# Optimization experiments

Hardware: AMD Instinct MI355X
Metric: run time of the kernel (lower is better)

## Reference

```python
import jax, jax.numpy as jnp
import numpy as np

E, D, H = 1024, 64, 16   # embed_dim, head_dim, num_heads
B, L = 8, 4096


def _ln(x, g, b, eps=1e-5):
    m = jnp.mean(x, axis=-1, keepdims=True)
    v = jnp.var(x, axis=-1, keepdims=True)
    return (x - m) / jnp.sqrt(v + eps) * g + b


def setup_inputs() -> dict:
    key = jax.random.key(0)
    ks = jax.random.split(key, 10)
    s_e = 1.0 / np.sqrt(E)
    s_d = 1.0 / np.sqrt(D)
    f32 = jnp.float32
    return {
        "emb": jax.random.normal(ks[0], (B, L, E), f32),
        # per-head linears stacked on a leading head axis
        "Wa": jax.random.normal(ks[1], (H, E, D), f32) * s_e,
        "ba": jnp.zeros((H, D), f32),
        "Wb": jax.random.normal(ks[2], (H, E, D), f32) * s_e,
        "bb": jnp.zeros((H, D), f32),
        "Wc": jax.random.normal(ks[3], (H, D, D), f32) * s_d,
        "bc": jnp.zeros((H, D), f32),
        "head_w": jnp.ones((H,), f32),
        "hn_g": jnp.ones((H, D), f32),
        "hn_b": jnp.zeros((H, D), f32),
        "Wd": jax.random.normal(ks[4], (E, D), f32) * s_e,
        "bd": jnp.zeros((D,), f32),
        "W1": jax.random.normal(ks[5], (D, 4 * D), f32) * s_d,
        "b1": jnp.zeros((4 * D,), f32),
        "W2": jax.random.normal(ks[6], (4 * D, D), f32) * (1.0 / np.sqrt(4 * D)),
        "b2": jnp.zeros((D,), f32),
        "Wp": jax.random.normal(ks[7], (D, D), f32) * s_d,
        "bp": jnp.zeros((D,), f32),
        "ng": jnp.ones((D,), f32),
        "nb": jnp.zeros((D,), f32),
    }


def reference(emb, Wa, ba, Wb, bb, Wc, bc, head_w, hn_g, hn_b,
              Wd, bd, W1, b1, W2, b2, Wp, bp, ng, nb):
    b_sz, seq_len, _ = emb.shape
    n_heads, d_head = ba.shape

    # gates depend only on x_t -> precompute for all t, all heads  [B,L,H,D]
    a = jnp.tanh(jnp.einsum('ble,hed->blhd', emb, Wa) + ba)
    bt = jnp.einsum('ble,hed->blhd', emb, Wb) + bb

    # linear recurrence h_t = a_t * h_{t-1} + b_t over time
    a_t = jnp.moveaxis(a, 1, 0)    # [L,B,H,D]
    b_t = jnp.moveaxis(bt, 1, 0)

    def step(h, ab):
        at, btt = ab
        h = at * h + btt
        return h, h

    h0 = jnp.zeros((b_sz, n_heads, d_head), emb.dtype)
    _, hs = jax.lax.scan(step, h0, (a_t, b_t))
    hs = jnp.moveaxis(hs, 0, 1)    # [B,L,H,D]

    dx = emb @ Wd + bd             # [B,L,D] shared D(x_t)

    out = jnp.einsum('blhd,hde->blhe', hs, Wc) + bc + dx[:, :, None, :]
    out = _ln(out, hn_g, hn_b)     # per-head LayerNorm, gamma/beta [H,D]

    sum_heads = dx + jnp.einsum('h,blhd->bld', head_w, out)
    z = sum_heads / n_heads

    u = z + _ln(z, ng, nb)
    ffn = jax.nn.gelu(u @ W1 + b1, approximate=False) @ W2 + b2
    h_out = u + ffn
    return h_out @ Wp + bp
```

## Files before the change

### kernel.cpp

```cpp
#include <hip/hip_runtime.h>
#include <hip/hip_bf16.h>
#include <math.h>
#include <stdint.h>

#define E_DIM 1024
#define D_DIM 64
#define H_DIM 16
#define B_SZ  8
#define L_SEQ 4096
#define M_TOK (B_SZ * L_SEQ)
#define NCAT  2112
#define NPAD  2304
#define CHUNK 64
#define NCHUNK (L_SEQ / CHUNK)

typedef float  f32x4  __attribute__((ext_vector_type(4)));
typedef __bf16 bf16x8 __attribute__((ext_vector_type(8)));
typedef __bf16 bf16x4 __attribute__((ext_vector_type(4)));

__device__ __forceinline__ float tanh_fast(float v) {
  float vc = fminf(fmaxf(v, -12.f), 12.f);
  float ex = __expf(vc + vc);
  return (ex - 1.f) / (ex + 1.f);
}
__device__ __forceinline__ void load_lds16(const void* g, void* l) {
  __builtin_amdgcn_global_load_lds(
      (const __attribute__((address_space(1))) void*)g,
      (__attribute__((address_space(3))) void*)l, 16, 0, 0);
}

__global__ __launch_bounds__(256) void cast_emb(const float* __restrict__ in,
                                                bf16x4* __restrict__ out) {
  int i = blockIdx.x * 256 + threadIdx.x;
  float4 v = ((const float4*)in)[i];
  bf16x4 o;
  o[0] = (__bf16)v.x; o[1] = (__bf16)v.y; o[2] = (__bf16)v.z; o[3] = (__bf16)v.w;
  out[i] = o;
}

__global__ __launch_bounds__(256) void pack_w(
    const float* __restrict__ Wa, const float* __restrict__ ba,
    const float* __restrict__ Wb, const float* __restrict__ bb,
    const float* __restrict__ Wd, const float* __restrict__ bd,
    __bf16* __restrict__ wcat, float* __restrict__ bias) {
  int gid = blockIdx.x * 256 + threadIdx.x;
  int n = gid >> 10, k = gid & 1023;
  float w, bv;
  if (n < 1024) {
    int h = n >> 6, d = n & 63;
    w = Wa[((h << 10) | k) * 64 + d]; bv = ba[n];
  } else if (n < 2048) {
    int nn = n - 1024; int h = nn >> 6, d = nn & 63;
    w = Wb[((h << 10) | k) * 64 + d]; bv = bb[nn];
  } else if (n < NCAT) {
    int d = n - 2048;
    w = Wd[k * 64 + d];  bv = bd[d];
  } else { w = 0.f; bv = 0.f; }
  wcat[n * 1024 + k] = (__bf16)w;
  if (k == 0) bias[n] = bv;
}

__global__ __launch_bounds__(256) void pack_ffnw(
    const float* __restrict__ W1, const float* __restrict__ W2,
    const float* __restrict__ Wp,
    __bf16* __restrict__ g_w1t, __bf16* __restrict__ g_w2t,
    __bf16* __restrict__ g_wpt) {
  int idx = blockIdx.x * 256 + threadIdx.x;
  if (idx < 16384) {
    int k = idx >> 8, n = idx & 255;
    g_w1t[n * 72 + k] = (__bf16)W1[idx];
  } else if (idx < 32768) {
    int j = idx - 16384; int k = j >> 6, n = j & 63;
    g_w2t[n * 256 + (((k >> 3) ^ (n & 7)) << 3) + (k & 7)] = (__bf16)W2[j];
  } else {
    int j = idx - 32768; int k = j >> 6, n = j & 63;
    g_wpt[n * 72 + k] = (__bf16)Wp[j];
  }
}

__global__ __launch_bounds__(256) void pack_wct(const float* __restrict__ Wc,
                                                __bf16* __restrict__ wct) {
  int idx = blockIdx.x * 256 + threadIdx.x;
  int h = idx >> 12, e = (idx >> 6) & 63, d = idx & 63;
  wct[idx] = (__bf16)Wc[h * 4096 + d * 64 + e];
}

__global__ __launch_bounds__(512, 2) void gemm_fused(
    const __bf16* __restrict__ A, const __bf16* __restrict__ Wt,
    const float* __restrict__ bias,
    __bf16* __restrict__ abuf, __bf16* __restrict__ bbuf, float* __restrict__ dxbuf) {
  __shared__ __bf16 lds[65536];
  const int id = blockIdx.x;
  const int wg = (id & 7) * 144 + (id >> 3);
  const int mt = wg / 9, nt = wg % 9;
  const int m0 = mt * 256, n0 = nt * 256;
  const int t = threadIdx.x;
  const int w = t >> 6, l = t & 63;
  const int wr = w >> 2, wc = w & 3;
  const int q = l >> 4, c16 = l & 15;
  const int cp = q ^ ((c16 >> 1) & 3);
  const int srow = l >> 2;
  const int schk = (l & 3) ^ ((l >> 3) & 3);

  f32x4 acc[8][4];
#pragma unroll
  for (int i = 0; i < 8; ++i)
#pragma unroll
    for (int j = 0; j < 4; ++j) acc[i][j] = (f32x4)(0.f);

  auto stage = [&](int H) {
    int th = H >> 1, isB = H & 1, slot = th & 3;
    const __bf16* src = isB ? Wt : A;
    int base0 = isB ? n0 : m0;
    int ldsbase = (isB ? 32768 : 0) + slot * 8192;
#pragma unroll
    for (int r = 0; r < 2; ++r) {
      int rw = r * 128 + w * 16;
      load_lds16(src + (size_t)(base0 + rw + srow) * 1024 + th * 32 + schk * 8,
                 &lds[ldsbase + rw * 32]);
    }
  };

  auto tile_phases = [&](int tt, bool sA, bool sB) {
    const int slot = tt & 3;
    const __bf16* Asl = lds + slot * 8192;
    const __bf16* Bsl = lds + 32768 + slot * 8192;
    bf16x8 bfr[4], af[4];
#pragma unroll
    for (int j = 0; j < 4; ++j)
      bfr[j] = *(const bf16x8*)(Bsl + (wc * 64 + j * 16 + c16) * 32 + cp * 8);
#pragma unroll
    for (int i = 0; i < 4; ++i)
      af[i] = *(const bf16x8*)(Asl + (wr * 128 + i * 16 + c16) * 32 + cp * 8);
    if (sA) stage(2 * tt + 5);
    __builtin_amdgcn_s_setprio(1);
#pragma unroll
    for (int i = 0; i < 4; ++i)
#pragma unroll
      for (int j = 0; j < 4; ++j)
        acc[i][j] = __builtin_amdgcn_mfma_f32_16x16x32_bf16(af[i], bfr[j], acc[i][j], 0, 0, 0);
    __builtin_amdgcn_s_setprio(0);
    asm volatile("s_barrier" ::: "memory");
#pragma unroll
    for (int i = 0; i < 4; ++i)
      af[i] = *(const bf16x8*)(Asl + (wr * 128 + (4 + i) * 16 + c16) * 32 + cp * 8);
    if (sB) stage(2 * tt + 6);
    __builtin_amdgcn_s_setprio(1);
#pragma unroll
    for (int i = 0; i < 4; ++i)
#pragma unroll
      for (int j = 0; j < 4; ++j)
        acc[4 + i][j] = __builtin_amdgcn_mfma_f32_16x16x32_bf16(af[i], bfr[j], acc[4 + i][j], 0, 0, 0);
    __builtin_amdgcn_s_setprio(0);
  };

  stage(0); stage(1); stage(2); stage(3); stage(4);
  asm volatile("s_waitcnt vmcnt(6)" ::: "memory");
  asm volatile("s_barrier" ::: "memory");

#pragma unroll 1
  for (int tt = 0; tt < 29; ++tt) {
    tile_phases(tt, true, true);
    asm volatile("s_waitcnt vmcnt(6)" ::: "memory");
    asm volatile("s_barrier" ::: "memory");
  }
  tile_phases(29, true, false);
  asm volatile("s_waitcnt vmcnt(4)" ::: "memory");
  asm volatile("s_barrier" ::: "memory");
  tile_phases(30, false, false);
  asm volatile("s_waitcnt vmcnt(0)" ::: "memory");
  asm volatile("s_barrier" ::: "memory");
  tile_phases(31, false, false);

#pragma unroll
  for (int j = 0; j < 4; ++j) {
    int n = n0 + wc * 64 + j * 16 + c16;
    if (n >= NCAT) continue;
    float bv = bias[n];
#pragma unroll
    for (int i = 0; i < 8; ++i) {
      int mbase = m0 + wr * 128 + i * 16 + q * 4;
#pragma unroll
      for (int r = 0; r < 4; ++r) {
        float v = acc[i][j][r] + bv;
        int m = mbase + r;
        if (n < 1024)            abuf[(size_t)m * 1024 + n] = (__bf16)tanh_fast(v);
        else if (n < 2048)       bbuf[(size_t)m * 1024 + (n - 1024)] = (__bf16)v;
        else                     dxbuf[m * 64 + (n - 2048)] = v;
      }
    }
  }
}

__global__ __launch_bounds__(256) void scan_local_bf(
    __bf16* __restrict__ abuf, __bf16* __restrict__ bbuf,
    float* __restrict__ cA, float* __restrict__ cH) {
  int bc = blockIdx.x;
  int n4 = threadIdx.x * 4;
  size_t base = (size_t)bc * CHUNK * 1024 + n4;
  float p[4] = {1.f, 1.f, 1.f, 1.f}, h[4] = {0.f, 0.f, 0.f, 0.f};
#pragma unroll 4
  for (int s = 0; s < CHUNK; ++s) {
    size_t idx = base + (size_t)s * 1024;
    bf16x4 av = *(const bf16x4*)(abuf + idx);
    bf16x4 bv = *(const bf16x4*)(bbuf + idx);
    bf16x4 po, ho;
#pragma unroll
    for (int i = 0; i < 4; ++i) {
      float a = (float)av[i];
      p[i] *= a;
      h[i] = fmaf(a, h[i], (float)bv[i]);
      po[i] = (__bf16)p[i];
      ho[i] = (__bf16)h[i];
    }
    *(bf16x4*)(abuf + idx) = po;
    *(bf16x4*)(bbuf + idx) = ho;
  }
  int ci = bc * 1024 + n4;
  float4 pv = {p[0], p[1], p[2], p[3]};
  float4 hv = {h[0], h[1], h[2], h[3]};
  *(float4*)(cA + ci) = pv;
  *(float4*)(cH + ci) = hv;
}

__global__ __launch_bounds__(256) void scan_carry(
    const float* __restrict__ cA, const float* __restrict__ cH, float* __restrict__ cIn) {
  int gid = blockIdx.x * 256 + threadIdx.x;
  int n = gid & 1023, b = gid >> 10;
  float carry = 0.f;
  for (int c = 0; c < NCHUNK; ++c) {
    int idx = (b * NCHUNK + c) * 1024 + n;
    cIn[idx] = carry;
    carry = fmaf(cA[idx], carry, cH[idx]);
  }
}

__global__ __launch_bounds__(256) void heads_mfma(
    const __bf16* __restrict__ ahat, const __bf16* __restrict__ hloc,
    const float* __restrict__ dxbuf, const float* __restrict__ cIn,
    const __bf16* __restrict__ wct, const float* __restrict__ bch,
    const float* __restrict__ head_w, const float* __restrict__ hng,
    const float* __restrict__ hnb, const float* __restrict__ ng,
    const float* __restrict__ nbv, float* __restrict__ ubuf) {
  __shared__ float carryS[1024];
  const int tid = threadIdx.x, w = tid >> 6, l = tid & 63;
  const int q = l >> 4, c16 = l & 15;
  const int m0 = blockIdx.x * 64;
  const int b = m0 >> 12, c = (m0 & 4095) >> 6;
  const int cb = (b * NCHUNK + c) * 1024;
  ((float4*)carryS)[tid] = ((const float4*)(cIn + cb))[tid];
  __syncthreads();

  const size_t arow = (size_t)(m0 + w * 16 + c16) * 1024;

  float dxr[4][4];
#pragma unroll
  for (int j = 0; j < 4; ++j)
#pragma unroll
    for (int r = 0; r < 4; ++r)
      dxr[j][r] = dxbuf[(m0 + w * 16 + q * 4 + r) * 64 + j * 16 + c16];

  f32x4 accum[4];
#pragma unroll
  for (int j = 0; j < 4; ++j) accum[j] = (f32x4)(0.f);

  for (int h = 0; h < H_DIM; ++h) {
    bf16x8 af[2];
#pragma unroll
    for (int ks = 0; ks < 2; ++ks) {
      int dbase = h * 64 + ks * 32 + q * 8;
      bf16x8 av = *(const bf16x8*)(ahat + arow + dbase);
      bf16x8 hv = *(const bf16x8*)(hloc + arow + dbase);
      float4 cv0 = *(const float4*)(carryS + dbase);
      float4 cv1 = *(const float4*)(carryS + dbase + 4);
      bf16x8 hf;
      hf[0] = (__bf16)fmaf((float)av[0], cv0.x, (float)hv[0]);
      hf[1] = (__bf16)fmaf((float)av[1], cv0.y, (float)hv[1]);
      hf[2] = (__bf16)fmaf((float)av[2], cv0.z, (float)hv[2]);
      hf[3] = (__bf16)fmaf((float)av[3], cv0.w, (float)hv[3]);
      hf[4] = (__bf16)fmaf((float)av[4], cv1.x, (float)hv[4]);
      hf[5] = (__bf16)fmaf((float)av[5], cv1.y, (float)hv[5]);
      hf[6] = (__bf16)fmaf((float)av[6], cv1.z, (float)hv[6]);
      hf[7] = (__bf16)fmaf((float)av[7], cv1.w, (float)hv[7]);
      af[ks] = hf;
    }
    f32x4 acc[4];
#pragma unroll
    for (int j = 0; j < 4; ++j) acc[j] = (f32x4)(0.f);
#pragma unroll
    for (int ks = 0; ks < 2; ++ks)
#pragma unroll
      for (int j = 0; j < 4; ++j) {
        bf16x8 bf = *(const bf16x8*)(wct + h * 4096 + (j * 16 + c16) * 64 + ks * 32 + q * 8);
        acc[j] = __builtin_amdgcn_mfma_f32_16x16x32_bf16(af[ks], bf, acc[j], 0, 0, 0);
      }
    float hw = head_w[h];
    float g4[4], be4[4], bb4[4];
#pragma unroll
    for (int j = 0; j < 4; ++j) {
      int nh = h * 64 + j * 16 + c16;
      g4[j] = hng[nh]; bb4[j] = hnb[nh]; be4[j] = bch[nh];
    }
#pragma unroll
    for (int r = 0; r < 4; ++r) {
      float v0 = acc[0][r] + be4[0] + dxr[0][r];
      float v1 = acc[1][r] + be4[1] + dxr[1][r];
      float v2 = acc[2][r] + be4[2] + dxr[2][r];
      float v3 = acc[3][r] + be4[3] + dxr[3][r];
      float s  = (v0 + v1) + (v2 + v3);
      float s2 = fmaf(v0, v0, fmaf(v1, v1, fmaf(v2, v2, v3 * v3)));
#pragma unroll
      for (int off = 1; off < 16; off <<= 1) {
        s  += __shfl_xor(s, off, 64);
        s2 += __shfl_xor(s2, off, 64);
      }
      float mean = s * (1.f / 64.f);
      float var  = fmaf(s2, 1.f / 64.f, -mean * mean);
      float inv  = rsqrtf(fmaxf(var, 0.f) + 1e-5f);
      accum[0][r] = fmaf(hw, fmaf((v0 - mean) * inv, g4[0], bb4[0]), accum[0][r]);
      accum[1][r] = fmaf(hw, fmaf((v1 - mean) * inv, g4[1], bb4[1]), accum[1][r]);
      accum[2][r] = fmaf(hw, fmaf((v2 - mean) * inv, g4[2], bb4[2]), accum[2][r]);
      accum[3][r] = fmaf(hw, fmaf((v3 - mean) * inv, g4[3], bb4[3]), accum[3][r]);
    }
  }
  float ng4[4], nb4[4];
#pragma unroll
  for (int j = 0; j < 4; ++j) { ng4[j] = ng[j * 16 + c16]; nb4[j] = nbv[j * 16 + c16]; }
#pragma unroll
  for (int r = 0; r < 4; ++r) {
    float z0 = (dxr[0][r] + accum[0][r]) * (1.f / 16.f);
    float z1 = (dxr[1][r] + accum[1][r]) * (1.f / 16.f);
    float z2 = (dxr[2][r] + accum[2][r]) * (1.f / 16.f);
    float z3 = (dxr[3][r] + accum[3][r]) * (1.f / 16.f);
    float s  = (z0 + z1) + (z2 + z3);
    float s2 = fmaf(z0, z0, fmaf(z1, z1, fmaf(z2, z2, z3 * z3)));
#pragma unroll
    for (int off = 1; off < 16; off <<= 1) {
      s  += __shfl_xor(s, off, 64);
      s2 += __shfl_xor(s2, off, 64);
    }
    float mean = s * (1.f / 64.f);
    float var  = fmaf(s2, 1.f / 64.f, -mean * mean);
    float inv  = rsqrtf(fmaxf(var, 0.f) + 1e-5f);
    int mrow = (m0 + w * 16 + q * 4 + r) * 64;
    ubuf[mrow + 0 * 16 + c16] = z0 + fmaf((z0 - mean) * inv, ng4[0], nb4[0]);
    ubuf[mrow + 1 * 16 + c16] = z1 + fmaf((z1 - mean) * inv, ng4[1], nb4[1]);
    ubuf[mrow + 2 * 16 + c16] = z2 + fmaf((z2 - mean) * inv, ng4[2], nb4[2]);
    ubuf[mrow + 3 * 16 + c16] = z3 + fmaf((z3 - mean) * inv, ng4[3], nb4[3]);
  }
}

__global__ __launch_bounds__(256) void ffn_mfma(
    const float* __restrict__ ubuf,
    const __bf16* __restrict__ g_w1t, const __bf16* __restrict__ g_w2t,
    const __bf16* __restrict__ g_wpt,
    const float* __restrict__ b1, const float* __restrict__ b2,
    const float* __restrict__ bp, float* __restrict__ out) {
  __shared__ __bf16 pool[32768];
  const int tid = threadIdx.x, w = tid >> 6, l = tid & 63;
  const int q = l >> 4, c16 = l & 15;
  const int m0 = blockIdx.x * 64;
  __bf16* Us  = pool;
  __bf16* W1T = pool + 4608;
  __bf16* T1S = pool;
  __bf16* W2T = pool + 16384;
  __bf16* HoS = pool;
  __bf16* WpT = pool + 4608;

#pragma unroll
  for (int r = 0; r < 16; ++r) {
    int idx = r * 256 + tid, m = idx >> 6, e = idx & 63;
    Us[m * 72 + e] = (__bf16)ubuf[(size_t)(m0 + m) * 64 + e];
  }
#pragma unroll
  for (int r = 0; r < 9; ++r)
    load_lds16(g_w1t + (size_t)(r * 256 + tid) * 8,
               (char*)pool + 9216 + (r * 256 + w * 64) * 16);
  __syncthreads();

  f32x4 acc1[16];
#pragma unroll
  for (int j = 0; j < 16; ++j) acc1[j] = (f32x4)(0.f);
#pragma unroll
  for (int ks = 0; ks < 2; ++ks) {
    bf16x8 a = *(const bf16x8*)(Us + (w * 16 + c16) * 72 + ks * 32 + q * 8);
#pragma unroll
    for (int j = 0; j < 16; ++j) {
      bf16x8 b = *(const bf16x8*)(W1T + (j * 16 + c16) * 72 + ks * 32 + q * 8);
      acc1[j] = __builtin_amdgcn_mfma_f32_16x16x32_bf16(a, b, acc1[j], 0, 0, 0);
    }
  }
  __syncthreads();

#pragma unroll
  for (int r = 0; r < 8; ++r)
    load_lds16(g_w2t + (size_t)(r * 256 + tid) * 8,
               (char*)pool + 32768 + (r * 256 + w * 64) * 16);
#pragma unroll
  for (int j = 0; j < 16; ++j) {
    int n = j * 16 + c16;
    float bv = b1[n];
#pragma unroll
    for (int rr = 0; rr < 4; ++rr) {
      int m = w * 16 + q * 4 + rr;
      float x = acc1[j][rr] + bv;
      float g = 0.5f * x * (1.f + erff(x * 0.70710678118654752f));
      T1S[m * 256 + (((n >> 3) ^ (m & 7)) << 3) + (n & 7)] = (__bf16)g;
    }
  }
  __syncthreads();

  f32x4 acc2[4];
#pragma unroll
  for (int j = 0; j < 4; ++j) acc2[j] = (f32x4)(0.f);
  const int arow2 = w * 16 + c16;
#pragma unroll
  for (int ks = 0; ks < 8; ++ks) {
    bf16x8 a = *(const bf16x8*)(T1S + arow2 * 256 + (((ks * 4 + q) ^ (arow2 & 7)) << 3));
#pragma unroll
    for (int j = 0; j < 4; ++j) {
      int brow = j * 16 + c16;
      bf16x8 b = *(const bf16x8*)(W2T + brow * 256 + (((ks * 4 + q) ^ (brow & 7)) << 3));
      acc2[j] = __builtin_amdgcn_mfma_f32_16x16x32_bf16(a, b, acc2[j], 0, 0, 0);
    }
  }
  __syncthreads();

#pragma unroll
  for (int r = 0; r < 2; ++r)
    load_lds16(g_wpt + (size_t)(r * 256 + tid) * 8,
               (char*)pool + 9216 + (r * 256 + w * 64) * 16);
  if (tid < 64)
    load_lds16(g_wpt + (size_t)(512 + tid) * 8, (char*)pool + 9216 + 512 * 16);
#pragma unroll
  for (int j = 0; j < 4; ++j) {
    int e = j * 16 + c16;
    float bv = b2[e];
#pragma unroll
    for (int rr = 0; rr < 4; ++rr) {
      int m = w * 16 + q * 4 + rr;
      float hres = acc2[j][rr] + bv + ubuf[(size_t)(m0 + m) * 64 + e];
      HoS[m * 72 + e] = (__bf16)hres;
    }
  }
  __syncthreads();

  f32x4 acc3[4];
#pragma unroll
  for (int j = 0; j < 4; ++j) acc3[j] = (f32x4)(0.f);
#pragma unroll
  for (int ks = 0; ks < 2; ++ks) {
    bf16x8 a = *(const bf16x8*)(HoS + (w * 16 + c16) * 72 + ks * 32 + q * 8);
#pragma unroll
    for (int j = 0; j < 4; ++j) {
      bf16x8 b = *(const bf16x8*)(WpT + (j * 16 + c16) * 72 + ks * 32 + q * 8);
      acc3[j] = __builtin_amdgcn_mfma_f32_16x16x32_bf16(a, b, acc3[j], 0, 0, 0);
    }
  }
#pragma unroll
  for (int j = 0; j < 4; ++j) {
    int e = j * 16 + c16;
    float bv = bp[e];
#pragma unroll
    for (int rr = 0; rr < 4; ++rr) {
      int m = w * 16 + q * 4 + rr;
      out[(size_t)(m0 + m) * 64 + e] = acc3[j][rr] + bv;
    }
  }
}

extern "C" void kernel_launch(void* const* d_in, const int* in_sizes, int n_in,
                              void* d_out, int out_size, void* d_ws, size_t ws_size,
                              hipStream_t stream) {
  const float* emb    = (const float*)d_in[0];
  const float* Wa     = (const float*)d_in[1];
  const float* ba     = (const float*)d_in[2];
  const float* Wb     = (const float*)d_in[3];
  const float* bb     = (const float*)d_in[4];
  const float* Wc     = (const float*)d_in[5];
  const float* bc     = (const float*)d_in[6];
  const float* head_w = (const float*)d_in[7];
  const float* hn_g   = (const float*)d_in[8];
  const float* hn_b   = (const float*)d_in[9];
  const float* Wd     = (const float*)d_in[10];
  const float* bd     = (const float*)d_in[11];
  const float* W1     = (const float*)d_in[12];
  const float* b1     = (const float*)d_in[13];
  const float* W2     = (const float*)d_in[14];
  const float* b2     = (const float*)d_in[15];
  const float* Wp     = (const float*)d_in[16];
  const float* bp     = (const float*)d_in[17];
  const float* ng     = (const float*)d_in[18];
  const float* nb     = (const float*)d_in[19];
  float* out = (float*)d_out;

  char* wsp = (char*)d_ws;
  size_t off = 0;
  auto alloc = [&](size_t bytes) -> char* {
    char* p = wsp + off;
    off += (bytes + 255) & ~(size_t)255;
    return p;
  };
  __bf16* embh  = (__bf16*)alloc((size_t)M_TOK * E_DIM * 2);
  __bf16* wcat  = (__bf16*)alloc((size_t)NPAD * E_DIM * 2);
  float*  bias  = (float*)alloc((size_t)NPAD * 4);
  __bf16* abuf  = (__bf16*)alloc((size_t)M_TOK * 1024 * 2);
  __bf16* bbuf  = (__bf16*)alloc((size_t)M_TOK * 1024 * 2);
  float*  dxbuf = (float*)alloc((size_t)M_TOK * 64 * 4);
  float*  cA    = (float*)alloc((size_t)512 * 1024 * 4);
  float*  cH    = (float*)alloc((size_t)512 * 1024 * 4);
  float*  cIn   = (float*)alloc((size_t)512 * 1024 * 4);
  float*  ubuf  = (float*)alloc((size_t)M_TOK * 64 * 4);
  __bf16* g_w1t = (__bf16*)alloc((size_t)256 * 72 * 2);
  __bf16* g_w2t = (__bf16*)alloc((size_t)64 * 256 * 2);
  __bf16* g_wpt = (__bf16*)alloc((size_t)64 * 72 * 2);
  __bf16* wct   = (__bf16*)alloc((size_t)H_DIM * 64 * 64 * 2);

  cast_emb<<<dim3(32768), dim3(256), 0, stream>>>(emb, (bf16x4*)embh);
  pack_w<<<dim3(9216), dim3(256), 0, stream>>>(Wa, ba, Wb, bb, Wd, bd, wcat, bias);
  pack_ffnw<<<dim3(144), dim3(256), 0, stream>>>(W1, W2, Wp, g_w1t, g_w2t, g_wpt);
  pack_wct<<<dim3(256), dim3(256), 0, stream>>>(Wc, wct);
  gemm_fused<<<dim3(1152), dim3(512), 0, stream>>>(embh, wcat, bias, abuf, bbuf, dxbuf);
  scan_local_bf<<<dim3(512), dim3(256), 0, stream>>>(abuf, bbuf, cA, cH);
  scan_carry<<<dim3(32), dim3(256), 0, stream>>>(cA, cH, cIn);
  heads_mfma<<<dim3(512), dim3(256), 0, stream>>>(abuf, bbuf, dxbuf, cIn, wct, bc,
                                                  head_w, hn_g, hn_b, ng, nb, ubuf);
  ffn_mfma<<<dim3(512), dim3(256), 0, stream>>>(ubuf, g_w1t, g_w2t, g_wpt,
                                                b1, b2, bp, out);
}
```

Before: 600.5 us.

## Restructure fused GEMM main loop to K=64 tiles with four-phase double buffering

Reworks the LDS staging of the big fused projection GEMM. The K-tile grows from 32 to 64 with an 8-way XOR swizzle, and the buffers go from a 4-slot ring to double buffering split into half-tiles. Each K step runs as four phases that interleave half-tile global-to-LDS loads with MFMA on two row blocks, and each phase has explicit barriers and lgkmcnt/vmcnt waits. The aim is fewer loop iterations and better overlap of loads with MFMA, at the cost of more barriers per tile and a more fragile wait-count schedule.

```diff
diff --git a/kernel.cpp b/kernel.cpp
--- a/kernel.cpp
+++ b/kernel.cpp
@@ -98,9 +98,8 @@
   const int w = t >> 6, l = t & 63;
   const int wr = w >> 2, wc = w & 3;
   const int q = l >> 4, c16 = l & 15;
-  const int cp = q ^ ((c16 >> 1) & 3);
-  const int srow = l >> 2;
-  const int schk = (l & 3) ^ ((l >> 3) & 3);
+  const int cxor = c16 & 7;
+  const int schk = (l & 7) ^ ((l >> 3) & 7);
 
   f32x4 acc[8][4];
 #pragma unroll
@@ -108,69 +107,77 @@
 #pragma unroll
     for (int j = 0; j < 4; ++j) acc[i][j] = (f32x4)(0.f);
 
-  auto stage = [&](int H) {
-    int th = H >> 1, isB = H & 1, slot = th & 3;
+  auto stage = [&](int kt, int isB, int h) {
     const __bf16* src = isB ? Wt : A;
-    int base0 = isB ? n0 : m0;
-    int ldsbase = (isB ? 32768 : 0) + slot * 8192;
-#pragma unroll
-    for (int r = 0; r < 2; ++r) {
-      int rw = r * 128 + w * 16;
-      load_lds16(src + (size_t)(base0 + rw + srow) * 1024 + th * 32 + schk * 8,
-                 &lds[ldsbase + rw * 32]);
-    }
+    const int base0 = (isB ? n0 : m0) + h * 128 + w * 16;
+    __bf16* dst = lds + (isB ? 32768 : 0) + (((kt & 1) << 1) + h) * 8192 + w * 1024;
+#pragma unroll
+    for (int r = 0; r < 2; ++r)
+      load_lds16(src + (size_t)(base0 + r * 8 + (l >> 3)) * 1024 + kt * 64 + schk * 8,
+                 dst + r * 512);
   };
 
-  auto tile_phases = [&](int tt, bool sA, bool sB) {
-    const int slot = tt & 3;
-    const __bf16* Asl = lds + slot * 8192;
-    const __bf16* Bsl = lds + 32768 + slot * 8192;
-    bf16x8 bfr[4], af[4];
-#pragma unroll
-    for (int j = 0; j < 4; ++j)
-      bfr[j] = *(const bf16x8*)(Bsl + (wc * 64 + j * 16 + c16) * 32 + cp * 8);
-#pragma unroll
-    for (int i = 0; i < 4; ++i)
-      af[i] = *(const bf16x8*)(Asl + (wr * 128 + i * 16 + c16) * 32 + cp * 8);
-    if (sA) stage(2 * tt + 5);
+  auto ldA = [&](int d, int i, int ks) -> bf16x8 {
+    return *(const bf16x8*)(lds + ((d << 1) + wr) * 8192 + (i * 16 + c16) * 64 +
+                            (((ks << 2) + q) ^ cxor) * 8);
+  };
+  auto ldB = [&](int d, int j, int ks) -> bf16x8 {
+    return *(const bf16x8*)(lds + 32768 + ((d << 1) + (wc >> 1)) * 8192 +
+                            ((wc & 1) * 64 + j * 16 + c16) * 64 +
+                            (((ks << 2) + q) ^ cxor) * 8);
+  };
+
+  bf16x8 bfr[4][2];
+
+  auto phase = [&](int d, int i0, bool loadB, bool do_stage, int skt, int sisB,
+                   int sh, int wait) {
+    if (loadB) {
+#pragma unroll
+      for (int j = 0; j < 4; ++j) {
+        bfr[j][0] = ldB(d, j, 0);
+        bfr[j][1] = ldB(d, j, 1);
+      }
+    }
+    bf16x8 a00 = ldA(d, i0, 0), a01 = ldA(d, i0, 1);
+    bf16x8 a10 = ldA(d, i0 + 1, 0), a11 = ldA(d, i0 + 1, 1);
+    if (do_stage) stage(skt, sisB, sh);
+    __builtin_amdgcn_sched_barrier(0);
+    __builtin_amdgcn_s_barrier();
+    asm volatile("s_waitcnt lgkmcnt(0)" ::: "memory");
+    __builtin_amdgcn_sched_barrier(0);
     __builtin_amdgcn_s_setprio(1);
 #pragma unroll
-    for (int i = 0; i < 4; ++i)
+    for (int ks = 0; ks < 2; ++ks) {
+      const bf16x8 a0 = ks ? a01 : a00;
+      const bf16x8 a1 = ks ? a11 : a10;
 #pragma unroll
       for (int j = 0; j < 4; ++j)
-        acc[i][j] = __builtin_amdgcn_mfma_f32_16x16x32_bf16(af[i], bfr[j], acc[i][j], 0, 0, 0);
+        acc[i0][j] = __builtin_amdgcn_mfma_f32_16x16x32_bf16(a0, bfr[j][ks], acc[i0][j], 0, 0, 0);
+#pragma unroll
+      for (int j = 0; j < 4; ++j)
+        acc[i0 + 1][j] = __builtin_amdgcn_mfma_f32_16x16x32_bf16(a1, bfr[j][ks], acc[i0 + 1][j], 0, 0, 0);
+    }
     __builtin_amdgcn_s_setprio(0);
-    asm volatile("s_barrier" ::: "memory");
-#pragma unroll
-    for (int i = 0; i < 4; ++i)
-      af[i] = *(const bf16x8*)(Asl + (wr * 128 + (4 + i) * 16 + c16) * 32 + cp * 8);
-    if (sB) stage(2 * tt + 6);
-    __builtin_amdgcn_s_setprio(1);
-#pragma unroll
-    for (int i = 0; i < 4; ++i)
-#pragma unroll
-      for (int j = 0; j < 4; ++j)
-        acc[4 + i][j] = __builtin_amdgcn_mfma_f32_16x16x32_bf16(af[i], bfr[j], acc[4 + i][j], 0, 0, 0);
-    __builtin_amdgcn_s_setprio(0);
+    __builtin_amdgcn_sched_barrier(0);
+    if (wait == 0)      asm volatile("s_waitcnt vmcnt(0)" ::: "memory");
+    else if (wait == 4) asm volatile("s_waitcnt vmcnt(4)" ::: "memory");
+    __builtin_amdgcn_s_barrier();
   };
 
-  stage(0); stage(1); stage(2); stage(3); stage(4);
-  asm volatile("s_waitcnt vmcnt(6)" ::: "memory");
-  asm volatile("s_barrier" ::: "memory");
-
-#pragma unroll 1
-  for (int tt = 0; tt < 29; ++tt) {
-    tile_phases(tt, true, true);
-    asm volatile("s_waitcnt vmcnt(6)" ::: "memory");
-    asm volatile("s_barrier" ::: "memory");
-  }
-  tile_phases(29, true, false);
+  stage(0, 0, 0); stage(0, 0, 1); stage(0, 1, 0); stage(0, 1, 1);
+  stage(1, 1, 0); stage(1, 1, 1);
   asm volatile("s_waitcnt vmcnt(4)" ::: "memory");
-  asm volatile("s_barrier" ::: "memory");
-  tile_phases(30, false, false);
-  asm volatile("s_waitcnt vmcnt(0)" ::: "memory");
-  asm volatile("s_barrier" ::: "memory");
-  tile_phases(31, false, false);
+  __builtin_amdgcn_s_barrier();
+
+#pragma unroll 2
+  for (int tt = 0; tt < 16; ++tt) {
+    const int d = tt & 1;
+    const bool s1 = (tt + 1) < 16, s2 = (tt + 2) < 16;
+    phase(d, 0, true,  s1, tt + 1, 0, 0, -1);
+    phase(d, 2, false, s1, tt + 1, 0, 1, -1);
+    phase(d, 4, false, s2, tt + 2, 1, 0, -1);
+    phase(d, 6, false, s2, tt + 2, 1, 1, (tt < 14) ? 4 : (tt == 14 ? 0 : -1));
+  }
 
 #pragma unroll
   for (int j = 0; j < 4; ++j) {
```

Result: no change. 605.6 us (+0.9%).
